# Performance work log

Hardware: AMD Instinct MI355X
Metric: run time of the kernel (lower is better)

Reference implementation:

```python
import jax, jax.numpy as jnp
import numpy as np

B, N, D = 16, 2048, 256  # batch (pairs*2), num_keypoints, descriptor_dim


def setup_inputs() -> dict:
    key = jax.random.key(0)
    k1, k2, k3, k4 = jax.random.split(key, 4)
    descriptors = jax.random.normal(k1, (B, N, D), dtype=jnp.float32)
    mask = jax.random.randint(k2, (B, N), 0, 2, dtype=jnp.int32)
    proj_w = jax.random.normal(k3, (D, D), dtype=jnp.float32) * 0.02
    proj_b = jnp.zeros((D,), dtype=jnp.float32)
    match_w = jax.random.normal(k4, (1, D), dtype=jnp.float32) * 0.02
    match_b = jnp.zeros((1,), dtype=jnp.float32)
    return {"descriptors": descriptors, "mask": mask, "proj_w": proj_w,
            "proj_b": proj_b, "match_w": match_w, "match_b": match_b}


def reference(descriptors, mask, proj_w, proj_b, match_w, match_b):
    batch, n, d = descriptors.shape
    pairs = batch // 2
    # final projection + temperature scaling
    m_desc = (descriptors @ proj_w.T + proj_b) / jnp.asarray(d, descriptors.dtype) ** 0.25
    m_desc = m_desc.reshape(pairs, 2, n, d)
    # similarity: [pairs, n0, n1]
    similarity = jnp.einsum('bnd,bmd->bnm', m_desc[:, 0], m_desc[:, 1])
    mask_p = mask.reshape(pairs, 2, n)
    pair_mask = mask_p[:, 0][:, :, None] * mask_p[:, 1][:, None, :]
    neg_min = jnp.finfo(similarity.dtype).min
    similarity = jnp.where(pair_mask == 0, neg_min, similarity)
    # matchability logits: [B, n, 1] -> split per pair
    matchability = (descriptors @ match_w.T + match_b).reshape(pairs, 2, n)
    m0 = matchability[:, 0]  # [pairs, n]
    m1 = matchability[:, 1]  # [pairs, n]
    certainties = jax.nn.log_sigmoid(m0)[:, :, None] + jax.nn.log_sigmoid(m1)[:, None, :]
    scores0 = jax.nn.log_softmax(similarity, axis=2)
    scores1 = jax.nn.log_softmax(similarity, axis=1)
    inner = scores0 + scores1 + certainties
    scores = jnp.zeros((pairs, n + 1, n + 1), dtype=similarity.dtype)
    scores = scores.at[:, :n, :n].set(inner)
    scores = scores.at[:, :-1, -1].set(jax.nn.log_sigmoid(-m0))
    scores = scores.at[:, -1, :-1].set(jax.nn.log_sigmoid(-m1))
    return scores
```

## Files before the change

### kernel.cpp

```cpp
#include <hip/hip_runtime.h>
#include <math.h>

typedef unsigned short u16;
typedef __attribute__((ext_vector_type(8))) short bf16x8;
typedef __attribute__((ext_vector_type(4))) float f32x4;

#define N 2048
#define D 256
#define PAIRS 8
#define NO 2049
#define NEGMIN  -3.40282347e38f
#define MASKVAL -3.0e38f
#define LDA 72
#define LDST 136

#define WS_LS0   0
#define WS_LS1   (1*PAIRS*N)
#define WS_LSN0  (2*PAIRS*N)
#define WS_LSN1  (3*PAIRS*N)
#define WS_CST   (6*PAIRS*N)
#define WS_RPM   (8*PAIRS*N)
#define WS_RPS   (WS_RPM + PAIRS*16*N)
#define WS_CPM   (WS_RPS + PAIRS*16*N)
#define WS_CPS   (WS_CPM + PAIRS*16*N)
#define WS_ROW   (WS_CPS + PAIRS*16*N)
#define WS_F_COUNT (WS_ROW + 4*PAIRS*N)

__device__ __forceinline__ float b2f(u16 u) {
    return __uint_as_float(((unsigned)u) << 16);
}
__device__ __forceinline__ u16 f2b(float f) {
    unsigned x = __float_as_uint(f);
    x += 0x7FFFu + ((x >> 16) & 1u);
    return (u16)(x >> 16);
}
__device__ __forceinline__ unsigned pk2(float a, float b) {
    return (unsigned)f2b(a) | ((unsigned)f2b(b) << 16);
}
__device__ __forceinline__ float logsig(float x) {
    return fminf(x, 0.f) - log1pf(expf(-fabsf(x)));
}
__device__ __forceinline__ void onmerge(float& m, float& s, float om, float os) {
    float nm = fmaxf(m, om);
    s = s * __expf(m - nm) + os * __expf(om - nm);
    m = nm;
}
__device__ __forceinline__ void gl_lds16(const u16* g, u16* l) {
    __builtin_amdgcn_global_load_lds(
        (const __attribute__((address_space(1))) unsigned*)(const void*)g,
        (__attribute__((address_space(3))) unsigned*)(void*)l, 16, 0, 0);
}

__global__ __launch_bounds__(256) void k_proj_mfma(const float* __restrict__ A,
                                                   const float* __restrict__ W,
                                                   const float* __restrict__ bias,
                                                   const float* __restrict__ mw,
                                                   const float* __restrict__ mb,
                                                   u16* __restrict__ mdesc,
                                                   float* __restrict__ wsf) {
    __shared__ union {
        struct { u16 A[128 * LDA]; u16 B[128 * LDA]; } t;
        u16 stage[128][LDST];
    } sh;
    int r0 = blockIdx.x * 128, c0 = blockIdx.y * 128;
    int tid = threadIdx.x;
    int w = tid >> 6, lane = tid & 63;
    int ln = lane & 15, q = lane >> 4;
    int wr0 = (w >> 1) * 64, wc0 = (w & 1) * 64;
    f32x4 zero = {0.f, 0.f, 0.f, 0.f};
    f32x4 acc[4][4];
    #pragma unroll
    for (int a = 0; a < 4; ++a)
        #pragma unroll
        for (int b = 0; b < 4; ++b) acc[a][b] = zero;
    float mdot[4] = {0.f, 0.f, 0.f, 0.f};
    int domatch = (blockIdx.y == 0);

    for (int kb = 0; kb < D; kb += 64) {
        __syncthreads();
        #pragma unroll
        for (int t = 0; t < 4; ++t) {
            int c = t * 256 + tid;
            int row = c >> 3, part = c & 7;
            const float* ap = A + (size_t)(r0 + row) * D + kb + part * 8;
            float4 f0 = *(const float4*)ap;
            float4 f1 = *(const float4*)(ap + 4);
            uint4 va;
            va.x = pk2(f0.x, f0.y); va.y = pk2(f0.z, f0.w);
            va.z = pk2(f1.x, f1.y); va.w = pk2(f1.z, f1.w);
            *(uint4*)&sh.t.A[row * LDA + part * 8] = va;
            if (domatch) {
                float4 w0 = *(const float4*)(mw + kb + part * 8);
                float4 w1 = *(const float4*)(mw + kb + part * 8 + 4);
                mdot[t] += f0.x*w0.x + f0.y*w0.y + f0.z*w0.z + f0.w*w0.w
                         + f1.x*w1.x + f1.y*w1.y + f1.z*w1.z + f1.w*w1.w;
            }
            const float* bp = W + (size_t)(c0 + row) * D + kb + part * 8;
            float4 g0 = *(const float4*)bp;
            float4 g1 = *(const float4*)(bp + 4);
            uint4 vb;
            vb.x = pk2(g0.x, g0.y); vb.y = pk2(g0.z, g0.w);
            vb.z = pk2(g1.x, g1.y); vb.w = pk2(g1.z, g1.w);
            *(uint4*)&sh.t.B[row * LDA + part * 8] = vb;
        }
        __syncthreads();
        #pragma unroll
        for (int kk = 0; kk < 64; kk += 32) {
            bf16x8 af[4], bf[4];
            #pragma unroll
            for (int ri = 0; ri < 4; ++ri)
                af[ri] = *(const bf16x8*)&sh.t.A[(wr0 + ri*16 + ln) * LDA + kk + q*8];
            #pragma unroll
            for (int ci = 0; ci < 4; ++ci)
                bf[ci] = *(const bf16x8*)&sh.t.B[(wc0 + ci*16 + ln) * LDA + kk + q*8];
            #pragma unroll
            for (int ri = 0; ri < 4; ++ri)
                #pragma unroll
                for (int ci = 0; ci < 4; ++ci)
                    acc[ri][ci] = __builtin_amdgcn_mfma_f32_16x16x32_bf16(af[ri], bf[ci], acc[ri][ci], 0, 0, 0);
        }
    }
    if (domatch) {
        #pragma unroll
        for (int t = 0; t < 4; ++t) {
            float s = mdot[t];
            s += __shfl_xor(s, 1, 64);
            s += __shfl_xor(s, 2, 64);
            s += __shfl_xor(s, 4, 64);
            if ((tid & 7) == 0) {
                int row_g = r0 + t * 32 + (tid >> 3);
                float m = s + mb[0];
                int b = row_g >> 11;
                int i = row_g & (N - 1);
                int pp = b >> 1, sid = b & 1;
                float ls = logsig(m), lsn = logsig(-m);
                if (sid == 0) { wsf[WS_LS0 + pp*N + i] = ls; wsf[WS_LSN0 + pp*N + i] = lsn; }
                else          { wsf[WS_LS1 + pp*N + i] = ls; wsf[WS_LSN1 + pp*N + i] = lsn; }
            }
        }
    }
    __syncthreads();
    #pragma unroll
    for (int ri = 0; ri < 4; ++ri) {
        #pragma unroll
        for (int reg = 0; reg < 4; ++reg) {
            int row_l = wr0 + ri*16 + q*4 + reg;
            #pragma unroll
            for (int ci = 0; ci < 4; ++ci) {
                int col = c0 + wc0 + ci*16 + ln;
                float v = (acc[ri][ci][reg] + bias[col]) * 0.25f;
                sh.stage[row_l][wc0 + ci*16 + ln] = f2b(v);
            }
        }
    }
    __syncthreads();
    {
        int row_l = tid >> 1, half = tid & 1;
        u16* dp = mdesc + (size_t)(r0 + row_l) * D + c0 + half * 64;
        const u16* lp = &sh.stage[row_l][half * 64];
        #pragma unroll
        for (int i = 0; i < 8; ++i)
            *(uint4*)(dp + i * 8) = *(const uint4*)(lp + i * 8);
    }
}

__global__ __launch_bounds__(256) void k_sim_mfma(const u16* __restrict__ mdesc,
                                                  const int* __restrict__ mask,
                                                  u16* __restrict__ sim,
                                                  float* __restrict__ wsf) {
    __shared__ union {
        u16 lds[4][128 * 64];
        u16 stage[128][LDST];
    } sh;
    __shared__ float rpm[128][2], rps[128][2];
    __shared__ float cpm[128][2], cps[128][2];
    int p = blockIdx.z;
    const u16* Am = mdesc + (size_t)(2*p) * N * D;
    const u16* Bm = mdesc + (size_t)(2*p + 1) * N * D;
    int r0 = blockIdx.x * 128, c0 = blockIdx.y * 128;
    int tid = threadIdx.x;
    int w = tid >> 6, lane = tid & 63;
    int ln = lane & 15, q = lane >> 4;
    int wr0 = (w >> 1) * 64, wc0 = (w & 1) * 64;
    int rsub = lane >> 3;
    int scol = (((lane & 7) ^ rsub) << 3);
    f32x4 zero = {0.f, 0.f, 0.f, 0.f};
    f32x4 acc[4][4];
    #pragma unroll
    for (int a = 0; a < 4; ++a)
        #pragma unroll
        for (int b = 0; b < 4; ++b) acc[a][b] = zero;

    #define STAGE(t_, bufi_) do {                                               \
        int kb_ = (t_) * 64;                                                    \
        u16* Ad_ = &sh.lds[(bufi_)*2][0];                                       \
        u16* Bd_ = &sh.lds[(bufi_)*2+1][0];                                     \
        _Pragma("unroll")                                                       \
        for (int j_ = 0; j_ < 4; ++j_) {                                        \
            int row_ = w * 32 + j_ * 8 + rsub;                                  \
            gl_lds16(Am + (size_t)(r0 + row_) * D + kb_ + scol,                 \
                     Ad_ + (w * 32 + j_ * 8) * 64);                             \
            gl_lds16(Bm + (size_t)(c0 + row_) * D + kb_ + scol,                 \
                     Bd_ + (w * 32 + j_ * 8) * 64);                             \
        }                                                                       \
    } while (0)

    STAGE(0, 0);
    __syncthreads();
    #pragma unroll
    for (int t = 0; t < 4; ++t) {
        int cur = t & 1;
        if (t < 3) STAGE(t + 1, cur ^ 1);
        const char* Abase = (const char*)&sh.lds[cur*2][0];
        const char* Bbase = (const char*)&sh.lds[cur*2+1][0];
        #pragma unroll
        for (int kk = 0; kk < 64; kk += 32) {
            bf16x8 af[4], bf[4];
            int cbase = kk * 2 + q * 16;
            int cswz = cbase ^ ((ln & 7) << 4);
            #pragma unroll
            for (int ri = 0; ri < 4; ++ri) {
                int row = wr0 + ri*16 + ln;
                af[ri] = *(const bf16x8*)(Abase + row * 128 + cswz);
            }
            #pragma unroll
            for (int ci = 0; ci < 4; ++ci) {
                int row = wc0 + ci*16 + ln;
                bf[ci] = *(const bf16x8*)(Bbase + row * 128 + cswz);
            }
            #pragma unroll
            for (int ri = 0; ri < 4; ++ri)
                #pragma unroll
                for (int ci = 0; ci < 4; ++ci)
                    acc[ri][ci] = __builtin_amdgcn_mfma_f32_16x16x32_bf16(af[ri], bf[ci], acc[ri][ci], 0, 0, 0);
        }
        __syncthreads();
    }
    #undef STAGE

    const int* m0 = mask + (size_t)(2*p) * N;
    const int* m1 = mask + (size_t)(2*p + 1) * N;
    int mcol[4];
    #pragma unroll
    for (int ci = 0; ci < 4; ++ci) mcol[ci] = m1[c0 + wc0 + ci*16 + ln];
    #pragma unroll
    for (int ri = 0; ri < 4; ++ri) {
        #pragma unroll
        for (int reg = 0; reg < 4; ++reg) {
            int row_l = wr0 + ri*16 + q*4 + reg;
            int mr = m0[r0 + row_l];
            #pragma unroll
            for (int ci = 0; ci < 4; ++ci) {
                float v = (mr && mcol[ci]) ? acc[ri][ci][reg] : MASKVAL;
                acc[ri][ci][reg] = v;
                sh.stage[row_l][wc0 + ci*16 + ln] = f2b(v);
            }
        }
    }
    #pragma unroll
    for (int ri = 0; ri < 4; ++ri) {
        #pragma unroll
        for (int reg = 0; reg < 4; ++reg) {
            float x0 = acc[ri][0][reg], x1 = acc[ri][1][reg];
            float x2 = acc[ri][2][reg], x3 = acc[ri][3][reg];
            float m = fmaxf(fmaxf(x0, x1), fmaxf(x2, x3));
            #pragma unroll
            for (int off = 1; off <= 8; off <<= 1)
                m = fmaxf(m, __shfl_xor(m, off, 64));
            float s = __expf(x0 - m) + __expf(x1 - m) + __expf(x2 - m) + __expf(x3 - m);
            #pragma unroll
            for (int off = 1; off <= 8; off <<= 1)
                s += __shfl_xor(s, off, 64);
            if (ln == 0) {
                int rl = wr0 + ri*16 + q*4 + reg;
                rpm[rl][w & 1] = m; rps[rl][w & 1] = s;
            }
        }
    }
    #pragma unroll
    for (int ci = 0; ci < 4; ++ci) {
        float m = acc[0][ci][0];
        #pragma unroll
        for (int ri = 0; ri < 4; ++ri)
            #pragma unroll
            for (int reg = 0; reg < 4; ++reg)
                if (!(ri == 0 && reg == 0)) m = fmaxf(m, acc[ri][ci][reg]);
        #pragma unroll
        for (int off = 16; off <= 32; off <<= 1)
            m = fmaxf(m, __shfl_xor(m, off, 64));
        float s = 0.f;
        #pragma unroll
        for (int ri = 0; ri < 4; ++ri)
            #pragma unroll
            for (int reg = 0; reg < 4; ++reg)
                s += __expf(acc[ri][ci][reg] - m);
        #pragma unroll
        for (int off = 16; off <= 32; off <<= 1)
            s += __shfl_xor(s, off, 64);
        if (q == 0) {
            int cl = wc0 + ci*16 + ln;
            cpm[cl][w >> 1] = m; cps[cl][w >> 1] = s;
        }
    }
    __syncthreads();
    {
        int row_l = tid >> 1, half = tid & 1;
        u16* sp = sim + ((size_t)p * N + r0 + row_l) * N + c0 + half * 64;
        const u16* lp = &sh.stage[row_l][half * 64];
        #pragma unroll
        for (int i = 0; i < 8; ++i)
            *(uint4*)(sp + i * 8) = *(const uint4*)(lp + i * 8);
    }
    if (tid < 128) {
        float m = rpm[tid][0], s = rps[tid][0];
        onmerge(m, s, rpm[tid][1], rps[tid][1]);
        size_t o = (size_t)(p * 16 + blockIdx.y) * N + r0 + tid;
        wsf[WS_RPM + o] = m; wsf[WS_RPS + o] = s;
    } else {
        int c = tid - 128;
        float m = cpm[c][0], s = cps[c][0];
        onmerge(m, s, cpm[c][1], cps[c][1]);
        size_t o = (size_t)(p * 16 + blockIdx.x) * N + c0 + c;
        wsf[WS_CPM + o] = m;
        wsf[WS_CPS + o] = s;
    }
}

__global__ __launch_bounds__(256) void k_red(float* __restrict__ wsf) {
    int i = blockIdx.x * 256 + threadIdx.x;
    int p = blockIdx.y;
    float m = wsf[WS_CPM + (size_t)(p*16) * N + i];
    float s = wsf[WS_CPS + (size_t)(p*16) * N + i];
    #pragma unroll
    for (int rb = 1; rb < 16; ++rb)
        onmerge(m, s, wsf[WS_CPM + (size_t)(p*16 + rb) * N + i],
                      wsf[WS_CPS + (size_t)(p*16 + rb) * N + i]);
    float2 cpack;
    cpack.x = -m - logf(s);
    cpack.y = wsf[WS_LS1 + p*N + i];
    *(float2*)&wsf[WS_CST + ((size_t)p * N + i) * 2] = cpack;
    float rm = wsf[WS_RPM + (size_t)(p*16) * N + i];
    float rs = wsf[WS_RPS + (size_t)(p*16) * N + i];
    #pragma unroll
    for (int rb = 1; rb < 16; ++rb)
        onmerge(rm, rs, wsf[WS_RPM + (size_t)(p*16 + rb) * N + i],
                        wsf[WS_RPS + (size_t)(p*16 + rb) * N + i]);
    float4 rpack;
    rpack.x = -rm - logf(rs);
    rpack.y = wsf[WS_LS0  + p*N + i];
    rpack.z = wsf[WS_LSN0 + p*N + i];
    rpack.w = 0.f;
    *(float4*)&wsf[WS_ROW + ((size_t)p * N + i) * 4] = rpack;
}

__global__ __launch_bounds__(256) void k_final(u16* __restrict__ out,
                                               const u16* __restrict__ sim,
                                               const float* __restrict__ wsf) {
    int strip = blockIdx.x;
    int p = blockIdx.y;
    int tid = threadIdx.x;
    unsigned* up = (unsigned*)out;
    if (strip == 256) {
        int head = p & 1;
        size_t B0 = ((size_t)p * NO + N) * NO;
        size_t U0 = (B0 + head) >> 1;
        const float* lsn1 = wsf + WS_LSN1 + p * N;
        #pragma unroll
        for (int k = 0; k < 4; ++k) {
            int kk = k * 256 + tid;
            int j0 = head + 2 * kk;
            float o0 = (j0 < N) ? lsn1[j0] : 0.f;
            float o1 = (j0 + 1 < N) ? lsn1[j0 + 1] : 0.f;
            up[U0 + kk] = pk2(o0, o1);
        }
        if (tid == 0) {
            if (head) out[B0] = f2b(lsn1[0]);
            else      out[B0 + N] = 0;
        }
        return;
    }
    __shared__ u16 stg[8][2052];
    int c8 = tid * 8;
    const float* cst = wsf + WS_CST + ((size_t)p * N + c8) * 2;
    float4 cs[4];
    #pragma unroll
    for (int k = 0; k < 4; ++k) cs[k] = *(const float4*)(cst + 4 * k);
    #pragma unroll
    for (int r = 0; r < 8; ++r) {
        int i = strip * 8 + r;
        int head = (p + i) & 1;
        float4 rsv = *(const float4*)&wsf[WS_ROW + ((size_t)p * N + i) * 4];
        float rc = rsv.x, l0 = rsv.y, ln0 = rsv.z;
        uint4 v = *(const uint4*)(sim + ((size_t)p * N + i) * N + c8);
        unsigned vv[4] = {v.x, v.y, v.z, v.w};
        float o[8];
        #pragma unroll
        for (int k = 0; k < 8; ++k) {
            float x = b2f((u16)(vv[k >> 1] >> ((k & 1) * 16)));
            float cA = ((const float*)&cs[0])[2 * k];
            float s1 = ((const float*)&cs[0])[2 * k + 1];
            float t = (x + rc) + (x + cA);
            o[k] = fmaxf(fmaxf(t, MASKVAL) + (l0 + s1), MASKVAL);
        }
        if (!head) {
            uint4 wv;
            wv.x = pk2(o[0], o[1]); wv.y = pk2(o[2], o[3]);
            wv.z = pk2(o[4], o[5]); wv.w = pk2(o[6], o[7]);
            *(uint4*)&stg[r][c8] = wv;
        } else {
            stg[r][c8 + 1] = f2b(o[0]);
            *(unsigned*)&stg[r][c8 + 2] = pk2(o[1], o[2]);
            *(unsigned*)&stg[r][c8 + 4] = pk2(o[3], o[4]);
            *(unsigned*)&stg[r][c8 + 6] = pk2(o[5], o[6]);
            stg[r][c8 + 8] = f2b(o[7]);
        }
        if (tid == 255) stg[r][2048 + head] = f2b(ln0);
    }
    __syncthreads();
    #pragma unroll
    for (int r = 0; r < 8; ++r) {
        int i = strip * 8 + r;
        int head = (p + i) & 1;
        size_t B0 = ((size_t)p * NO + i) * NO;
        size_t U0 = (B0 + head) >> 1;
        const unsigned* srow32 = (const unsigned*)&stg[r][0];
        #pragma unroll
        for (int k = 0; k < 4; ++k) {
            int kk = k * 256 + tid;
            up[U0 + kk] = srow32[kk + head];
        }
        if (tid == 0) {
            if (head) out[B0] = stg[r][1];
            else      out[B0 + N] = stg[r][2048];
        }
    }
}

extern "C" void kernel_launch(void* const* d_in, const int* in_sizes, int n_in,
                              void* d_out, int out_size, void* d_ws, size_t ws_size,
                              hipStream_t stream) {
    const float* desc    = (const float*)d_in[0];
    const int*   mask    = (const int*)d_in[1];
    const float* proj_w  = (const float*)d_in[2];
    const float* proj_b  = (const float*)d_in[3];
    const float* match_w = (const float*)d_in[4];
    const float* match_b = (const float*)d_in[5];
    u16*   out = (u16*)d_out;
    float* wsf = (float*)d_ws;
    u16*   mdesc = (u16*)((char*)d_ws + (size_t)WS_F_COUNT * sizeof(float));
    u16*   simw  = mdesc + (size_t)16 * N * D;

    k_proj_mfma<<<dim3(256, 2),    256, 0, stream>>>(desc, proj_w, proj_b, match_w, match_b, mdesc, wsf);
    k_sim_mfma <<<dim3(16, 16, 8), 256, 0, stream>>>(mdesc, mask, simw, wsf);
    k_red      <<<dim3(8, 8),      256, 0, stream>>>(wsf);
    k_final    <<<dim3(257, 8),    256, 0, stream>>>(out, simw, wsf);
}
```

Before: 257.6 us.

## Fuse four kernels into one cooperative persistent kernel with grid syncs

Replaces the projection, similarity, reduction and final-write kernels with one persistent cooperative kernel. It loops over tiles per phase and separates the phases with grid-wide barriers. The sim GEMM also drops its double-buffered LDS staging in favour of single-buffer loads, so less LDS is used and more blocks can be resident. This removes launch gaps between kernels, but it adds grid sync cost, loses load/compute overlap in the sim phase, and ties the grid size to the occupancy query.

```diff
diff --git a/kernel.cpp b/kernel.cpp
--- a/kernel.cpp
+++ b/kernel.cpp
@@ -1,5 +1,8 @@
 #include <hip/hip_runtime.h>
+#include <hip/hip_cooperative_groups.h>
 #include <math.h>
+
+namespace cg = cooperative_groups;
 
 typedef unsigned short u16;
 typedef __attribute__((ext_vector_type(8))) short bf16x8;
@@ -9,7 +12,6 @@
 #define D 256
 #define PAIRS 8
 #define NO 2049
-#define NEGMIN  -3.40282347e38f
 #define MASKVAL -3.0e38f
 #define LDA 72
 #define LDST 136
@@ -51,133 +53,16 @@
         (__attribute__((address_space(3))) unsigned*)(void*)l, 16, 0, 0);
 }
 
-__global__ __launch_bounds__(256) void k_proj_mfma(const float* __restrict__ A,
-                                                   const float* __restrict__ W,
-                                                   const float* __restrict__ bias,
-                                                   const float* __restrict__ mw,
-                                                   const float* __restrict__ mb,
-                                                   u16* __restrict__ mdesc,
-                                                   float* __restrict__ wsf) {
-    __shared__ union {
-        struct { u16 A[128 * LDA]; u16 B[128 * LDA]; } t;
-        u16 stage[128][LDST];
-    } sh;
-    int r0 = blockIdx.x * 128, c0 = blockIdx.y * 128;
-    int tid = threadIdx.x;
-    int w = tid >> 6, lane = tid & 63;
-    int ln = lane & 15, q = lane >> 4;
-    int wr0 = (w >> 1) * 64, wc0 = (w & 1) * 64;
-    f32x4 zero = {0.f, 0.f, 0.f, 0.f};
-    f32x4 acc[4][4];
-    #pragma unroll
-    for (int a = 0; a < 4; ++a)
-        #pragma unroll
-        for (int b = 0; b < 4; ++b) acc[a][b] = zero;
-    float mdot[4] = {0.f, 0.f, 0.f, 0.f};
-    int domatch = (blockIdx.y == 0);
-
-    for (int kb = 0; kb < D; kb += 64) {
-        __syncthreads();
-        #pragma unroll
-        for (int t = 0; t < 4; ++t) {
-            int c = t * 256 + tid;
-            int row = c >> 3, part = c & 7;
-            const float* ap = A + (size_t)(r0 + row) * D + kb + part * 8;
-            float4 f0 = *(const float4*)ap;
-            float4 f1 = *(const float4*)(ap + 4);
-            uint4 va;
-            va.x = pk2(f0.x, f0.y); va.y = pk2(f0.z, f0.w);
-            va.z = pk2(f1.x, f1.y); va.w = pk2(f1.z, f1.w);
-            *(uint4*)&sh.t.A[row * LDA + part * 8] = va;
-            if (domatch) {
-                float4 w0 = *(const float4*)(mw + kb + part * 8);
-                float4 w1 = *(const float4*)(mw + kb + part * 8 + 4);
-                mdot[t] += f0.x*w0.x + f0.y*w0.y + f0.z*w0.z + f0.w*w0.w
-                         + f1.x*w1.x + f1.y*w1.y + f1.z*w1.z + f1.w*w1.w;
-            }
-            const float* bp = W + (size_t)(c0 + row) * D + kb + part * 8;
-            float4 g0 = *(const float4*)bp;
-            float4 g1 = *(const float4*)(bp + 4);
-            uint4 vb;
-            vb.x = pk2(g0.x, g0.y); vb.y = pk2(g0.z, g0.w);
-            vb.z = pk2(g1.x, g1.y); vb.w = pk2(g1.z, g1.w);
-            *(uint4*)&sh.t.B[row * LDA + part * 8] = vb;
-        }
-        __syncthreads();
-        #pragma unroll
-        for (int kk = 0; kk < 64; kk += 32) {
-            bf16x8 af[4], bf[4];
-            #pragma unroll
-            for (int ri = 0; ri < 4; ++ri)
-                af[ri] = *(const bf16x8*)&sh.t.A[(wr0 + ri*16 + ln) * LDA + kk + q*8];
-            #pragma unroll
-            for (int ci = 0; ci < 4; ++ci)
-                bf[ci] = *(const bf16x8*)&sh.t.B[(wc0 + ci*16 + ln) * LDA + kk + q*8];
-            #pragma unroll
-            for (int ri = 0; ri < 4; ++ri)
-                #pragma unroll
-                for (int ci = 0; ci < 4; ++ci)
-                    acc[ri][ci] = __builtin_amdgcn_mfma_f32_16x16x32_bf16(af[ri], bf[ci], acc[ri][ci], 0, 0, 0);
-        }
-    }
-    if (domatch) {
-        #pragma unroll
-        for (int t = 0; t < 4; ++t) {
-            float s = mdot[t];
-            s += __shfl_xor(s, 1, 64);
-            s += __shfl_xor(s, 2, 64);
-            s += __shfl_xor(s, 4, 64);
-            if ((tid & 7) == 0) {
-                int row_g = r0 + t * 32 + (tid >> 3);
-                float m = s + mb[0];
-                int b = row_g >> 11;
-                int i = row_g & (N - 1);
-                int pp = b >> 1, sid = b & 1;
-                float ls = logsig(m), lsn = logsig(-m);
-                if (sid == 0) { wsf[WS_LS0 + pp*N + i] = ls; wsf[WS_LSN0 + pp*N + i] = lsn; }
-                else          { wsf[WS_LS1 + pp*N + i] = ls; wsf[WS_LSN1 + pp*N + i] = lsn; }
-            }
-        }
-    }
-    __syncthreads();
-    #pragma unroll
-    for (int ri = 0; ri < 4; ++ri) {
-        #pragma unroll
-        for (int reg = 0; reg < 4; ++reg) {
-            int row_l = wr0 + ri*16 + q*4 + reg;
-            #pragma unroll
-            for (int ci = 0; ci < 4; ++ci) {
-                int col = c0 + wc0 + ci*16 + ln;
-                float v = (acc[ri][ci][reg] + bias[col]) * 0.25f;
-                sh.stage[row_l][wc0 + ci*16 + ln] = f2b(v);
-            }
-        }
-    }
-    __syncthreads();
-    {
-        int row_l = tid >> 1, half = tid & 1;
-        u16* dp = mdesc + (size_t)(r0 + row_l) * D + c0 + half * 64;
-        const u16* lp = &sh.stage[row_l][half * 64];
-        #pragma unroll
-        for (int i = 0; i < 8; ++i)
-            *(uint4*)(dp + i * 8) = *(const uint4*)(lp + i * 8);
-    }
-}
-
-__global__ __launch_bounds__(256) void k_sim_mfma(const u16* __restrict__ mdesc,
-                                                  const int* __restrict__ mask,
-                                                  u16* __restrict__ sim,
-                                                  float* __restrict__ wsf) {
-    __shared__ union {
-        u16 lds[4][128 * 64];
-        u16 stage[128][LDST];
-    } sh;
-    __shared__ float rpm[128][2], rps[128][2];
-    __shared__ float cpm[128][2], cps[128][2];
-    int p = blockIdx.z;
-    const u16* Am = mdesc + (size_t)(2*p) * N * D;
-    const u16* Bm = mdesc + (size_t)(2*p + 1) * N * D;
-    int r0 = blockIdx.x * 128, c0 = blockIdx.y * 128;
+__global__ __launch_bounds__(256, 4) void k_mega(
+        const float* __restrict__ desc, const int* __restrict__ mask,
+        const float* __restrict__ W, const float* __restrict__ bias,
+        const float* __restrict__ mw, const float* __restrict__ mb,
+        u16* __restrict__ out, float* __restrict__ wsf,
+        u16* __restrict__ mdesc, u16* __restrict__ simw) {
+    cg::grid_group gg = cg::this_grid();
+    __shared__ __align__(16) u16 buf[18432];
+    __shared__ float redf[128][8];
+    const int G = gridDim.x;
     int tid = threadIdx.x;
     int w = tid >> 6, lane = tid & 63;
     int ln = lane & 15, q = lane >> 4;
@@ -185,254 +70,347 @@
     int rsub = lane >> 3;
     int scol = (((lane & 7) ^ rsub) << 3);
     f32x4 zero = {0.f, 0.f, 0.f, 0.f};
-    f32x4 acc[4][4];
-    #pragma unroll
-    for (int a = 0; a < 4; ++a)
-        #pragma unroll
-        for (int b = 0; b < 4; ++b) acc[a][b] = zero;
-
-    #define STAGE(t_, bufi_) do {                                               \
-        int kb_ = (t_) * 64;                                                    \
-        u16* Ad_ = &sh.lds[(bufi_)*2][0];                                       \
-        u16* Bd_ = &sh.lds[(bufi_)*2+1][0];                                     \
-        _Pragma("unroll")                                                       \
-        for (int j_ = 0; j_ < 4; ++j_) {                                        \
-            int row_ = w * 32 + j_ * 8 + rsub;                                  \
-            gl_lds16(Am + (size_t)(r0 + row_) * D + kb_ + scol,                 \
-                     Ad_ + (w * 32 + j_ * 8) * 64);                             \
-            gl_lds16(Bm + (size_t)(c0 + row_) * D + kb_ + scol,                 \
-                     Bd_ + (w * 32 + j_ * 8) * 64);                             \
-        }                                                                       \
-    } while (0)
-
-    STAGE(0, 0);
-    __syncthreads();
-    #pragma unroll
-    for (int t = 0; t < 4; ++t) {
-        int cur = t & 1;
-        if (t < 3) STAGE(t + 1, cur ^ 1);
-        const char* Abase = (const char*)&sh.lds[cur*2][0];
-        const char* Bbase = (const char*)&sh.lds[cur*2+1][0];
-        #pragma unroll
-        for (int kk = 0; kk < 64; kk += 32) {
-            bf16x8 af[4], bf[4];
-            int cbase = kk * 2 + q * 16;
-            int cswz = cbase ^ ((ln & 7) << 4);
-            #pragma unroll
-            for (int ri = 0; ri < 4; ++ri) {
-                int row = wr0 + ri*16 + ln;
-                af[ri] = *(const bf16x8*)(Abase + row * 128 + cswz);
-            }
-            #pragma unroll
-            for (int ci = 0; ci < 4; ++ci) {
-                int row = wc0 + ci*16 + ln;
-                bf[ci] = *(const bf16x8*)(Bbase + row * 128 + cswz);
-            }
+
+    for (int tt = blockIdx.x; tt < 512; tt += G) {
+        int r0 = (tt & 255) * 128, c0 = (tt >> 8) * 128;
+        int domatch = (tt < 256);
+        u16* As = buf;
+        u16* Bs = buf + 128 * LDA;
+        f32x4 acc[4][4];
+        #pragma unroll
+        for (int a = 0; a < 4; ++a)
+            #pragma unroll
+            for (int b = 0; b < 4; ++b) acc[a][b] = zero;
+        float mdot[4] = {0.f, 0.f, 0.f, 0.f};
+        for (int kb = 0; kb < D; kb += 64) {
+            __syncthreads();
+            #pragma unroll
+            for (int t = 0; t < 4; ++t) {
+                int c = t * 256 + tid;
+                int row = c >> 3, part = c & 7;
+                const float* ap = desc + (size_t)(r0 + row) * D + kb + part * 8;
+                float4 f0 = *(const float4*)ap;
+                float4 f1 = *(const float4*)(ap + 4);
+                uint4 va;
+                va.x = pk2(f0.x, f0.y); va.y = pk2(f0.z, f0.w);
+                va.z = pk2(f1.x, f1.y); va.w = pk2(f1.z, f1.w);
+                *(uint4*)&As[row * LDA + part * 8] = va;
+                if (domatch) {
+                    float4 w0 = *(const float4*)(mw + kb + part * 8);
+                    float4 w1 = *(const float4*)(mw + kb + part * 8 + 4);
+                    mdot[t] += f0.x*w0.x + f0.y*w0.y + f0.z*w0.z + f0.w*w0.w
+                             + f1.x*w1.x + f1.y*w1.y + f1.z*w1.z + f1.w*w1.w;
+                }
+                const float* bp = W + (size_t)(c0 + row) * D + kb + part * 8;
+                float4 g0 = *(const float4*)bp;
+                float4 g1 = *(const float4*)(bp + 4);
+                uint4 vb;
+                vb.x = pk2(g0.x, g0.y); vb.y = pk2(g0.z, g0.w);
+                vb.z = pk2(g1.x, g1.y); vb.w = pk2(g1.z, g1.w);
+                *(uint4*)&Bs[row * LDA + part * 8] = vb;
+            }
+            __syncthreads();
+            #pragma unroll
+            for (int kk = 0; kk < 64; kk += 32) {
+                bf16x8 af[4], bfr[4];
+                #pragma unroll
+                for (int ri = 0; ri < 4; ++ri)
+                    af[ri] = *(const bf16x8*)&As[(wr0 + ri*16 + ln) * LDA + kk + q*8];
+                #pragma unroll
+                for (int ci = 0; ci < 4; ++ci)
+                    bfr[ci] = *(const bf16x8*)&Bs[(wc0 + ci*16 + ln) * LDA + kk + q*8];
+                #pragma unroll
+                for (int ri = 0; ri < 4; ++ri)
+                    #pragma unroll
+                    for (int ci = 0; ci < 4; ++ci)
+                        acc[ri][ci] = __builtin_amdgcn_mfma_f32_16x16x32_bf16(af[ri], bfr[ci], acc[ri][ci], 0, 0, 0);
+            }
+        }
+        if (domatch) {
+            #pragma unroll
+            for (int t = 0; t < 4; ++t) {
+                float s = mdot[t];
+                s += __shfl_xor(s, 1, 64);
+                s += __shfl_xor(s, 2, 64);
+                s += __shfl_xor(s, 4, 64);
+                if ((tid & 7) == 0) {
+                    int row_g = r0 + t * 32 + (tid >> 3);
+                    float m = s + mb[0];
+                    int b = row_g >> 11;
+                    int i = row_g & (N - 1);
+                    int pp = b >> 1, sid = b & 1;
+                    float ls = logsig(m), lsn = logsig(-m);
+                    if (sid == 0) { wsf[WS_LS0 + pp*N + i] = ls; wsf[WS_LSN0 + pp*N + i] = lsn; }
+                    else          { wsf[WS_LS1 + pp*N + i] = ls; wsf[WS_LSN1 + pp*N + i] = lsn; }
+                }
+            }
+        }
+        __syncthreads();
+        float bs[4];
+        #pragma unroll
+        for (int ci = 0; ci < 4; ++ci) bs[ci] = bias[c0 + wc0 + ci*16 + ln];
+        #pragma unroll
+        for (int ri = 0; ri < 4; ++ri) {
+            #pragma unroll
+            for (int reg = 0; reg < 4; ++reg) {
+                int row_l = wr0 + ri*16 + q*4 + reg;
+                #pragma unroll
+                for (int ci = 0; ci < 4; ++ci) {
+                    float v = (acc[ri][ci][reg] + bs[ci]) * 0.25f;
+                    buf[row_l * LDST + wc0 + ci*16 + ln] = f2b(v);
+                }
+            }
+        }
+        __syncthreads();
+        {
+            int row_l = tid >> 1, half = tid & 1;
+            u16* dp = mdesc + (size_t)(r0 + row_l) * D + c0 + half * 64;
+            const u16* lp = &buf[row_l * LDST + half * 64];
+            #pragma unroll
+            for (int i = 0; i < 8; ++i)
+                *(uint4*)(dp + i * 8) = *(const uint4*)(lp + i * 8);
+        }
+        __syncthreads();
+    }
+    gg.sync();
+
+    for (int tt = blockIdx.x; tt < 2048; tt += G) {
+        int p = tt >> 8;
+        int bx = (tt >> 4) & 15, by = tt & 15;
+        int r0 = bx * 128, c0 = by * 128;
+        const u16* Am = mdesc + (size_t)(2*p) * N * D;
+        const u16* Bm = mdesc + (size_t)(2*p + 1) * N * D;
+        u16* At = buf;
+        u16* Bt = buf + 8192;
+        f32x4 acc[4][4];
+        #pragma unroll
+        for (int a = 0; a < 4; ++a)
+            #pragma unroll
+            for (int b = 0; b < 4; ++b) acc[a][b] = zero;
+        for (int kb = 0; kb < D; kb += 64) {
+            #pragma unroll
+            for (int j = 0; j < 4; ++j) {
+                int row = w * 32 + j * 8 + rsub;
+                gl_lds16(Am + (size_t)(r0 + row) * D + kb + scol, At + (w * 32 + j * 8) * 64);
+                gl_lds16(Bm + (size_t)(c0 + row) * D + kb + scol, Bt + (w * 32 + j * 8) * 64);
+            }
+            __syncthreads();
+            #pragma unroll
+            for (int kk = 0; kk < 64; kk += 32) {
+                bf16x8 af[4], bfr[4];
+                int cswz = (kk * 2 + q * 16) ^ ((ln & 7) << 4);
+                #pragma unroll
+                for (int ri = 0; ri < 4; ++ri)
+                    af[ri] = *(const bf16x8*)((const char*)At + (wr0 + ri*16 + ln) * 128 + cswz);
+                #pragma unroll
+                for (int ci = 0; ci < 4; ++ci)
+                    bfr[ci] = *(const bf16x8*)((const char*)Bt + (wc0 + ci*16 + ln) * 128 + cswz);
+                #pragma unroll
+                for (int ri = 0; ri < 4; ++ri)
+                    #pragma unroll
+                    for (int ci = 0; ci < 4; ++ci)
+                        acc[ri][ci] = __builtin_amdgcn_mfma_f32_16x16x32_bf16(af[ri], bfr[ci], acc[ri][ci], 0, 0, 0);
+            }
+            __syncthreads();
+        }
+        const int* m0 = mask + (size_t)(2*p) * N;
+        const int* m1 = mask + (size_t)(2*p + 1) * N;
+        int mcol[4];
+        #pragma unroll
+        for (int ci = 0; ci < 4; ++ci) mcol[ci] = m1[c0 + wc0 + ci*16 + ln];
+        #pragma unroll
+        for (int ri = 0; ri < 4; ++ri) {
+            #pragma unroll
+            for (int reg = 0; reg < 4; ++reg) {
+                int row_l = wr0 + ri*16 + q*4 + reg;
+                int mr = m0[r0 + row_l];
+                #pragma unroll
+                for (int ci = 0; ci < 4; ++ci) {
+                    float v = (mr && mcol[ci]) ? acc[ri][ci][reg] : MASKVAL;
+                    acc[ri][ci][reg] = v;
+                    buf[row_l * LDST + wc0 + ci*16 + ln] = f2b(v);
+                }
+            }
+        }
+        #pragma unroll
+        for (int ri = 0; ri < 4; ++ri) {
+            #pragma unroll
+            for (int reg = 0; reg < 4; ++reg) {
+                float x0 = acc[ri][0][reg], x1 = acc[ri][1][reg];
+                float x2 = acc[ri][2][reg], x3 = acc[ri][3][reg];
+                float m = fmaxf(fmaxf(x0, x1), fmaxf(x2, x3));
+                #pragma unroll
+                for (int off = 1; off <= 8; off <<= 1)
+                    m = fmaxf(m, __shfl_xor(m, off, 64));
+                float s = __expf(x0 - m) + __expf(x1 - m) + __expf(x2 - m) + __expf(x3 - m);
+                #pragma unroll
+                for (int off = 1; off <= 8; off <<= 1)
+                    s += __shfl_xor(s, off, 64);
+                if (ln == 0) {
+                    int rl = wr0 + ri*16 + q*4 + reg;
+                    redf[rl][w & 1] = m; redf[rl][2 + (w & 1)] = s;
+                }
+            }
+        }
+        #pragma unroll
+        for (int ci = 0; ci < 4; ++ci) {
+            float m = acc[0][ci][0];
             #pragma unroll
             for (int ri = 0; ri < 4; ++ri)
                 #pragma unroll
-                for (int ci = 0; ci < 4; ++ci)
-                    acc[ri][ci] = __builtin_amdgcn_mfma_f32_16x16x32_bf16(af[ri], bf[ci], acc[ri][ci], 0, 0, 0);
+                for (int reg = 0; reg < 4; ++reg)
+                    if (!(ri == 0 && reg == 0)) m = fmaxf(m, acc[ri][ci][reg]);
+            #pragma unroll
+            for (int off = 16; off <= 32; off <<= 1)
+                m = fmaxf(m, __shfl_xor(m, off, 64));
+            float s = 0.f;
+            #pragma unroll
+            for (int ri = 0; ri < 4; ++ri)
+                #pragma unroll
+                for (int reg = 0; reg < 4; ++reg)
+                    s += __expf(acc[ri][ci][reg] - m);
+            #pragma unroll
+            for (int off = 16; off <= 32; off <<= 1)
+                s += __shfl_xor(s, off, 64);
+            if (q == 0) {
+                int cl = wc0 + ci*16 + ln;
+                redf[cl][4 + (w >> 1)] = m; redf[cl][6 + (w >> 1)] = s;
+            }
+        }
+        __syncthreads();
+        {
+            int row_l = tid >> 1, half = tid & 1;
+            u16* sp = simw + ((size_t)p * N + r0 + row_l) * N + c0 + half * 64;
+            const u16* lp = &buf[row_l * LDST + half * 64];
+            #pragma unroll
+            for (int i = 0; i < 8; ++i)
+                *(uint4*)(sp + i * 8) = *(const uint4*)(lp + i * 8);
+        }
+        if (tid < 128) {
+            float m = redf[tid][0], s = redf[tid][2];
+            onmerge(m, s, redf[tid][1], redf[tid][3]);
+            size_t o = (size_t)(p * 16 + by) * N + r0 + tid;
+            wsf[WS_RPM + o] = m; wsf[WS_RPS + o] = s;
+        } else {
+            int c = tid - 128;
+            float m = redf[c][4], s = redf[c][6];
+            onmerge(m, s, redf[c][5], redf[c][7]);
+            size_t o = (size_t)(p * 16 + bx) * N + c0 + c;
+            wsf[WS_CPM + o] = m;
+            wsf[WS_CPS + o] = s;
         }
         __syncthreads();
     }
-    #undef STAGE
-
-    const int* m0 = mask + (size_t)(2*p) * N;
-    const int* m1 = mask + (size_t)(2*p + 1) * N;
-    int mcol[4];
-    #pragma unroll
-    for (int ci = 0; ci < 4; ++ci) mcol[ci] = m1[c0 + wc0 + ci*16 + ln];
-    #pragma unroll
-    for (int ri = 0; ri < 4; ++ri) {
-        #pragma unroll
-        for (int reg = 0; reg < 4; ++reg) {
-            int row_l = wr0 + ri*16 + q*4 + reg;
-            int mr = m0[r0 + row_l];
-            #pragma unroll
-            for (int ci = 0; ci < 4; ++ci) {
-                float v = (mr && mcol[ci]) ? acc[ri][ci][reg] : MASKVAL;
-                acc[ri][ci][reg] = v;
-                sh.stage[row_l][wc0 + ci*16 + ln] = f2b(v);
-            }
-        }
+    gg.sync();
+
+    for (int u = blockIdx.x; u < 64; u += G) {
+        int p = u >> 3;
+        int i = (u & 7) * 256 + tid;
+        float m = wsf[WS_CPM + (size_t)(p*16) * N + i];
+        float s = wsf[WS_CPS + (size_t)(p*16) * N + i];
+        #pragma unroll
+        for (int rb = 1; rb < 16; ++rb)
+            onmerge(m, s, wsf[WS_CPM + (size_t)(p*16 + rb) * N + i],
+                          wsf[WS_CPS + (size_t)(p*16 + rb) * N + i]);
+        float2 cpack;
+        cpack.x = -m - logf(s);
+        cpack.y = wsf[WS_LS1 + p*N + i];
+        *(float2*)&wsf[WS_CST + ((size_t)p * N + i) * 2] = cpack;
+        float rm = wsf[WS_RPM + (size_t)(p*16) * N + i];
+        float rs = wsf[WS_RPS + (size_t)(p*16) * N + i];
+        #pragma unroll
+        for (int rb = 1; rb < 16; ++rb)
+            onmerge(rm, rs, wsf[WS_RPM + (size_t)(p*16 + rb) * N + i],
+                            wsf[WS_RPS + (size_t)(p*16 + rb) * N + i]);
+        float4 rpack;
+        rpack.x = -rm - logf(rs);
+        rpack.y = wsf[WS_LS0  + p*N + i];
+        rpack.z = wsf[WS_LSN0 + p*N + i];
+        rpack.w = 0.f;
+        *(float4*)&wsf[WS_ROW + ((size_t)p * N + i) * 4] = rpack;
     }
-    #pragma unroll
-    for (int ri = 0; ri < 4; ++ri) {
-        #pragma unroll
-        for (int reg = 0; reg < 4; ++reg) {
-            float x0 = acc[ri][0][reg], x1 = acc[ri][1][reg];
-            float x2 = acc[ri][2][reg], x3 = acc[ri][3][reg];
-            float m = fmaxf(fmaxf(x0, x1), fmaxf(x2, x3));
-            #pragma unroll
-            for (int off = 1; off <= 8; off <<= 1)
-                m = fmaxf(m, __shfl_xor(m, off, 64));
-            float s = __expf(x0 - m) + __expf(x1 - m) + __expf(x2 - m) + __expf(x3 - m);
-            #pragma unroll
-            for (int off = 1; off <= 8; off <<= 1)
-                s += __shfl_xor(s, off, 64);
-            if (ln == 0) {
-                int rl = wr0 + ri*16 + q*4 + reg;
-                rpm[rl][w & 1] = m; rps[rl][w & 1] = s;
-            }
-        }
-    }
-    #pragma unroll
-    for (int ci = 0; ci < 4; ++ci) {
-        float m = acc[0][ci][0];
-        #pragma unroll
-        for (int ri = 0; ri < 4; ++ri)
-            #pragma unroll
-            for (int reg = 0; reg < 4; ++reg)
-                if (!(ri == 0 && reg == 0)) m = fmaxf(m, acc[ri][ci][reg]);
-        #pragma unroll
-        for (int off = 16; off <= 32; off <<= 1)
-            m = fmaxf(m, __shfl_xor(m, off, 64));
-        float s = 0.f;
-        #pragma unroll
-        for (int ri = 0; ri < 4; ++ri)
-            #pragma unroll
-            for (int reg = 0; reg < 4; ++reg)
-                s += __expf(acc[ri][ci][reg] - m);
-        #pragma unroll
-        for (int off = 16; off <= 32; off <<= 1)
-            s += __shfl_xor(s, off, 64);
-        if (q == 0) {
-            int cl = wc0 + ci*16 + ln;
-            cpm[cl][w >> 1] = m; cps[cl][w >> 1] = s;
-        }
-    }
-    __syncthreads();
-    {
-        int row_l = tid >> 1, half = tid & 1;
-        u16* sp = sim + ((size_t)p * N + r0 + row_l) * N + c0 + half * 64;
-        const u16* lp = &sh.stage[row_l][half * 64];
-        #pragma unroll
-        for (int i = 0; i < 8; ++i)
-            *(uint4*)(sp + i * 8) = *(const uint4*)(lp + i * 8);
-    }
-    if (tid < 128) {
-        float m = rpm[tid][0], s = rps[tid][0];
-        onmerge(m, s, rpm[tid][1], rps[tid][1]);
-        size_t o = (size_t)(p * 16 + blockIdx.y) * N + r0 + tid;
-        wsf[WS_RPM + o] = m; wsf[WS_RPS + o] = s;
-    } else {
-        int c = tid - 128;
-        float m = cpm[c][0], s = cps[c][0];
-        onmerge(m, s, cpm[c][1], cps[c][1]);
-        size_t o = (size_t)(p * 16 + blockIdx.x) * N + c0 + c;
-        wsf[WS_CPM + o] = m;
-        wsf[WS_CPS + o] = s;
-    }
-}
-
-__global__ __launch_bounds__(256) void k_red(float* __restrict__ wsf) {
-    int i = blockIdx.x * 256 + threadIdx.x;
-    int p = blockIdx.y;
-    float m = wsf[WS_CPM + (size_t)(p*16) * N + i];
-    float s = wsf[WS_CPS + (size_t)(p*16) * N + i];
-    #pragma unroll
-    for (int rb = 1; rb < 16; ++rb)
-        onmerge(m, s, wsf[WS_CPM + (size_t)(p*16 + rb) * N + i],
-                      wsf[WS_CPS + (size_t)(p*16 + rb) * N + i]);
-    float2 cpack;
-    cpack.x = -m - logf(s);
-    cpack.y = wsf[WS_LS1 + p*N + i];
-    *(float2*)&wsf[WS_CST + ((size_t)p * N + i) * 2] = cpack;
-    float rm = wsf[WS_RPM + (size_t)(p*16) * N + i];
-    float rs = wsf[WS_RPS + (size_t)(p*16) * N + i];
-    #pragma unroll
-    for (int rb = 1; rb < 16; ++rb)
-        onmerge(rm, rs, wsf[WS_RPM + (size_t)(p*16 + rb) * N + i],
-                        wsf[WS_RPS + (size_t)(p*16 + rb) * N + i]);
-    float4 rpack;
-    rpack.x = -rm - logf(rs);
-    rpack.y = wsf[WS_LS0  + p*N + i];
-    rpack.z = wsf[WS_LSN0 + p*N + i];
-    rpack.w = 0.f;
-    *(float4*)&wsf[WS_ROW + ((size_t)p * N + i) * 4] = rpack;
-}
-
-__global__ __launch_bounds__(256) void k_final(u16* __restrict__ out,
-                                               const u16* __restrict__ sim,
-                                               const float* __restrict__ wsf) {
-    int strip = blockIdx.x;
-    int p = blockIdx.y;
-    int tid = threadIdx.x;
+    gg.sync();
+
     unsigned* up = (unsigned*)out;
-    if (strip == 256) {
-        int head = p & 1;
-        size_t B0 = ((size_t)p * NO + N) * NO;
-        size_t U0 = (B0 + head) >> 1;
-        const float* lsn1 = wsf + WS_LSN1 + p * N;
-        #pragma unroll
-        for (int k = 0; k < 4; ++k) {
-            int kk = k * 256 + tid;
-            int j0 = head + 2 * kk;
-            float o0 = (j0 < N) ? lsn1[j0] : 0.f;
-            float o1 = (j0 + 1 < N) ? lsn1[j0 + 1] : 0.f;
-            up[U0 + kk] = pk2(o0, o1);
-        }
-        if (tid == 0) {
-            if (head) out[B0] = f2b(lsn1[0]);
-            else      out[B0 + N] = 0;
-        }
-        return;
-    }
-    __shared__ u16 stg[8][2052];
-    int c8 = tid * 8;
-    const float* cst = wsf + WS_CST + ((size_t)p * N + c8) * 2;
-    float4 cs[4];
-    #pragma unroll
-    for (int k = 0; k < 4; ++k) cs[k] = *(const float4*)(cst + 4 * k);
-    #pragma unroll
-    for (int r = 0; r < 8; ++r) {
-        int i = strip * 8 + r;
-        int head = (p + i) & 1;
-        float4 rsv = *(const float4*)&wsf[WS_ROW + ((size_t)p * N + i) * 4];
-        float rc = rsv.x, l0 = rsv.y, ln0 = rsv.z;
-        uint4 v = *(const uint4*)(sim + ((size_t)p * N + i) * N + c8);
-        unsigned vv[4] = {v.x, v.y, v.z, v.w};
-        float o[8];
-        #pragma unroll
-        for (int k = 0; k < 8; ++k) {
-            float x = b2f((u16)(vv[k >> 1] >> ((k & 1) * 16)));
-            float cA = ((const float*)&cs[0])[2 * k];
-            float s1 = ((const float*)&cs[0])[2 * k + 1];
-            float t = (x + rc) + (x + cA);
-            o[k] = fmaxf(fmaxf(t, MASKVAL) + (l0 + s1), MASKVAL);
-        }
-        if (!head) {
-            uint4 wv;
-            wv.x = pk2(o[0], o[1]); wv.y = pk2(o[2], o[3]);
-            wv.z = pk2(o[4], o[5]); wv.w = pk2(o[6], o[7]);
-            *(uint4*)&stg[r][c8] = wv;
-        } else {
-            stg[r][c8 + 1] = f2b(o[0]);
-            *(unsigned*)&stg[r][c8 + 2] = pk2(o[1], o[2]);
-            *(unsigned*)&stg[r][c8 + 4] = pk2(o[3], o[4]);
-            *(unsigned*)&stg[r][c8 + 6] = pk2(o[5], o[6]);
-            stg[r][c8 + 8] = f2b(o[7]);
-        }
-        if (tid == 255) stg[r][2048 + head] = f2b(ln0);
-    }
-    __syncthreads();
-    #pragma unroll
-    for (int r = 0; r < 8; ++r) {
-        int i = strip * 8 + r;
-        int head = (p + i) & 1;
-        size_t B0 = ((size_t)p * NO + i) * NO;
-        size_t U0 = (B0 + head) >> 1;
-        const unsigned* srow32 = (const unsigned*)&stg[r][0];
-        #pragma unroll
-        for (int k = 0; k < 4; ++k) {
-            int kk = k * 256 + tid;
-            up[U0 + kk] = srow32[kk + head];
-        }
-        if (tid == 0) {
-            if (head) out[B0] = stg[r][1];
-            else      out[B0 + N] = stg[r][2048];
-        }
+    for (int u = blockIdx.x; u < PAIRS * 257; u += G) {
+        int p = u / 257;
+        int strip = u - p * 257;
+        if (strip == 256) {
+            int head = p & 1;
+            size_t B0 = ((size_t)p * NO + N) * NO;
+            size_t U0 = (B0 + head) >> 1;
+            const float* lsn1 = wsf + WS_LSN1 + p * N;
+            #pragma unroll
+            for (int k = 0; k < 4; ++k) {
+                int kk = k * 256 + tid;
+                int j0 = head + 2 * kk;
+                float o0 = (j0 < N) ? lsn1[j0] : 0.f;
+                float o1 = (j0 + 1 < N) ? lsn1[j0 + 1] : 0.f;
+                up[U0 + kk] = pk2(o0, o1);
+            }
+            if (tid == 0) {
+                if (head) out[B0] = f2b(lsn1[0]);
+                else      out[B0 + N] = 0;
+            }
+            continue;
+        }
+        int c8 = tid * 8;
+        const float* cst = wsf + WS_CST + ((size_t)p * N + c8) * 2;
+        float4 cs[4];
+        #pragma unroll
+        for (int k = 0; k < 4; ++k) cs[k] = *(const float4*)(cst + 4 * k);
+        #pragma unroll
+        for (int r = 0; r < 8; ++r) {
+            int i = strip * 8 + r;
+            int head = (p + i) & 1;
+            float4 rsv = *(const float4*)&wsf[WS_ROW + ((size_t)p * N + i) * 4];
+            float rc = rsv.x, l0 = rsv.y, ln0 = rsv.z;
+            uint4 v = *(const uint4*)(simw + ((size_t)p * N + i) * N + c8);
+            unsigned vv[4] = {v.x, v.y, v.z, v.w};
+            float o[8];
+            #pragma unroll
+            for (int k = 0; k < 8; ++k) {
+                float x = b2f((u16)(vv[k >> 1] >> ((k & 1) * 16)));
+                float cA = ((const float*)&cs[0])[2 * k];
+                float s1 = ((const float*)&cs[0])[2 * k + 1];
+                float t = (x + rc) + (x + cA);
+                o[k] = fmaxf(fmaxf(t, MASKVAL) + (l0 + s1), MASKVAL);
+            }
+            u16* stg = buf + r * 2052;
+            if (!head) {
+                uint4 wv;
+                wv.x = pk2(o[0], o[1]); wv.y = pk2(o[2], o[3]);
+                wv.z = pk2(o[4], o[5]); wv.w = pk2(o[6], o[7]);
+                *(uint4*)&stg[c8] = wv;
+            } else {
+                stg[c8 + 1] = f2b(o[0]);
+                *(unsigned*)&stg[c8 + 2] = pk2(o[1], o[2]);
+                *(unsigned*)&stg[c8 + 4] = pk2(o[3], o[4]);
+                *(unsigned*)&stg[c8 + 6] = pk2(o[5], o[6]);
+                stg[c8 + 8] = f2b(o[7]);
+            }
+            if (tid == 255) stg[2048 + head] = f2b(ln0);
+        }
+        __syncthreads();
+        #pragma unroll
+        for (int r = 0; r < 8; ++r) {
+            int i = strip * 8 + r;
+            int head = (p + i) & 1;
+            size_t B0 = ((size_t)p * NO + i) * NO;
+            size_t U0 = (B0 + head) >> 1;
+            const unsigned* srow32 = (const unsigned*)(buf + r * 2052);
+            #pragma unroll
+            for (int k = 0; k < 4; ++k) {
+                int kk = k * 256 + tid;
+                up[U0 + kk] = srow32[kk + head];
+            }
+            if (tid == 0) {
+                const u16* stg = buf + r * 2052;
+                if (head) out[B0] = stg[1];
+                else      out[B0 + N] = stg[2048];
+            }
+        }
+        __syncthreads();
     }
 }
 
@@ -450,8 +428,16 @@
     u16*   mdesc = (u16*)((char*)d_ws + (size_t)WS_F_COUNT * sizeof(float));
     u16*   simw  = mdesc + (size_t)16 * N * D;
 
-    k_proj_mfma<<<dim3(256, 2),    256, 0, stream>>>(desc, proj_w, proj_b, match_w, match_b, mdesc, wsf);
-    k_sim_mfma <<<dim3(16, 16, 8), 256, 0, stream>>>(mdesc, mask, simw, wsf);
-    k_red      <<<dim3(8, 8),      256, 0, stream>>>(wsf);
-    k_final    <<<dim3(257, 8),    256, 0, stream>>>(out, simw, wsf);
-}
+    static int nb = 0;
+    if (nb == 0) {
+        if (hipOccupancyMaxActiveBlocksPerMultiprocessor(&nb, k_mega, 256, 0) != hipSuccess || nb < 1)
+            nb = 1;
+        if (nb > 4) nb = 4;
+    }
+    int grid = nb * 256;
+
+    void* args[10] = { (void*)&desc, (void*)&mask, (void*)&proj_w, (void*)&proj_b,
+                       (void*)&match_w, (void*)&match_b, (void*)&out, (void*)&wsf,
+                       (void*)&mdesc, (void*)&simw };
+    hipLaunchCooperativeKernel((void*)k_mega, dim3(grid), dim3(256), args, 0, stream);
+}
```

Result: slower. 499.2 us (+93.8%).

## Replace double-buffered LDS staging with single buffer in similarity GEMM

Applied to the files above, without the earlier changes.

Removes the two-stage double-buffered global-to-LDS pipeline in the similarity MFMA kernel and uses a single A/B tile buffer, loaded then synchronised before each K step. This halves the kernel's LDS footprint (the union is now bounded by the epilogue stage array), which may allow more resident blocks per CU, but it gives up overlap of the next tile's loads with the current tile's MFMAs. The projection kernel also hoists the bias loads out of the epilogue loop into registers.

```diff
diff --git a/kernel.cpp b/kernel.cpp
--- a/kernel.cpp
+++ b/kernel.cpp
@@ -9,7 +9,6 @@
 #define D 256
 #define PAIRS 8
 #define NO 2049
-#define NEGMIN  -3.40282347e38f
 #define MASKVAL -3.0e38f
 #define LDA 72
 #define LDST 136
@@ -140,6 +139,9 @@
         }
     }
     __syncthreads();
+    float bs[4];
+    #pragma unroll
+    for (int ci = 0; ci < 4; ++ci) bs[ci] = bias[c0 + wc0 + ci*16 + ln];
     #pragma unroll
     for (int ri = 0; ri < 4; ++ri) {
         #pragma unroll
@@ -147,8 +149,7 @@
             int row_l = wr0 + ri*16 + q*4 + reg;
             #pragma unroll
             for (int ci = 0; ci < 4; ++ci) {
-                int col = c0 + wc0 + ci*16 + ln;
-                float v = (acc[ri][ci][reg] + bias[col]) * 0.25f;
+                float v = (acc[ri][ci][reg] + bs[ci]) * 0.25f;
                 sh.stage[row_l][wc0 + ci*16 + ln] = f2b(v);
             }
         }
@@ -169,7 +170,7 @@
                                                   u16* __restrict__ sim,
                                                   float* __restrict__ wsf) {
     __shared__ union {
-        u16 lds[4][128 * 64];
+        struct { u16 A[128 * 64]; u16 B[128 * 64]; } t;
         u16 stage[128][LDST];
     } sh;
     __shared__ float rpm[128][2], rps[128][2];
@@ -191,43 +192,24 @@
         #pragma unroll
         for (int b = 0; b < 4; ++b) acc[a][b] = zero;
 
-    #define STAGE(t_, bufi_) do {                                               \
-        int kb_ = (t_) * 64;                                                    \
-        u16* Ad_ = &sh.lds[(bufi_)*2][0];                                       \
-        u16* Bd_ = &sh.lds[(bufi_)*2+1][0];                                     \
-        _Pragma("unroll")                                                       \
-        for (int j_ = 0; j_ < 4; ++j_) {                                        \
-            int row_ = w * 32 + j_ * 8 + rsub;                                  \
-            gl_lds16(Am + (size_t)(r0 + row_) * D + kb_ + scol,                 \
-                     Ad_ + (w * 32 + j_ * 8) * 64);                             \
-            gl_lds16(Bm + (size_t)(c0 + row_) * D + kb_ + scol,                 \
-                     Bd_ + (w * 32 + j_ * 8) * 64);                             \
-        }                                                                       \
-    } while (0)
-
-    STAGE(0, 0);
-    __syncthreads();
-    #pragma unroll
-    for (int t = 0; t < 4; ++t) {
-        int cur = t & 1;
-        if (t < 3) STAGE(t + 1, cur ^ 1);
-        const char* Abase = (const char*)&sh.lds[cur*2][0];
-        const char* Bbase = (const char*)&sh.lds[cur*2+1][0];
+    for (int kb = 0; kb < D; kb += 64) {
+        #pragma unroll
+        for (int j = 0; j < 4; ++j) {
+            int row = w * 32 + j * 8 + rsub;
+            gl_lds16(Am + (size_t)(r0 + row) * D + kb + scol, &sh.t.A[(w * 32 + j * 8) * 64]);
+            gl_lds16(Bm + (size_t)(c0 + row) * D + kb + scol, &sh.t.B[(w * 32 + j * 8) * 64]);
+        }
+        __syncthreads();
         #pragma unroll
         for (int kk = 0; kk < 64; kk += 32) {
             bf16x8 af[4], bf[4];
-            int cbase = kk * 2 + q * 16;
-            int cswz = cbase ^ ((ln & 7) << 4);
-            #pragma unroll
-            for (int ri = 0; ri < 4; ++ri) {
-                int row = wr0 + ri*16 + ln;
-                af[ri] = *(const bf16x8*)(Abase + row * 128 + cswz);
-            }
-            #pragma unroll
-            for (int ci = 0; ci < 4; ++ci) {
-                int row = wc0 + ci*16 + ln;
-                bf[ci] = *(const bf16x8*)(Bbase + row * 128 + cswz);
-            }
+            int cswz = (kk * 2 + q * 16) ^ ((ln & 7) << 4);
+            #pragma unroll
+            for (int ri = 0; ri < 4; ++ri)
+                af[ri] = *(const bf16x8*)((const char*)sh.t.A + (wr0 + ri*16 + ln) * 128 + cswz);
+            #pragma unroll
+            for (int ci = 0; ci < 4; ++ci)
+                bf[ci] = *(const bf16x8*)((const char*)sh.t.B + (wc0 + ci*16 + ln) * 128 + cswz);
             #pragma unroll
             for (int ri = 0; ri < 4; ++ri)
                 #pragma unroll
@@ -236,8 +218,6 @@
         }
         __syncthreads();
     }
-    #undef STAGE
-
     const int* m0 = mask + (size_t)(2*p) * N;
     const int* m1 = mask + (size_t)(2*p + 1) * N;
     int mcol[4];
```

Result: faster. 250.5 us (-2.8%).
